# Optimization experiments

Hardware: AMD Instinct MI355X
Metric: run time of the kernel (lower is better)

## Reference

```python
import jax, jax.numpy as jnp
import numpy as np

N_NODES = 100000
N_EDGES = 1600000
IN_CH = 128
OUT_CH = 16
HEADS = 4
HID = HEADS * OUT_CH  # 64
OUT_SIZE = 4
NEG_SLOPE = 0.2


def _xavier(key, shape, fan_in, fan_out):
    bound = float(np.sqrt(6.0 / (fan_in + fan_out)))
    return jax.random.uniform(key, shape, jnp.float32, -bound, bound)


def setup_inputs() -> dict:
    key = jax.random.key(0)
    ks = jax.random.split(key, 32)
    inp = {
        "x": jax.random.normal(ks[0], (N_NODES, IN_CH), jnp.float32),
        "edge_index": jax.random.randint(ks[1], (2, N_EDGES), 0, N_NODES, jnp.int64),
    }
    cin = IN_CH
    for l in range(4):
        inp[f"W{l}"] = _xavier(ks[2 + 3 * l], (HID, cin), cin, HID)
        inp[f"b{l}"] = jnp.zeros((HID,), jnp.float32)
        inp[f"a{l}"] = _xavier(ks[3 + 3 * l], (HEADS, 2 * OUT_CH), 2 * OUT_CH, 1)
        cin = HID
    inp["fcW"] = _xavier(ks[20], (OUT_SIZE, HID), HID, OUT_SIZE)
    inp["fcb"] = jnp.zeros((OUT_SIZE,), jnp.float32)
    return inp


def _gat_layer(x, src, dst, W, b, att):
    n = x.shape[0]
    h = (x @ W.T + b).reshape(n, HEADS, OUT_CH)  # [N,H,C]
    # cat([x_i,x_j]) . att == (x_i . att[:, :C]) + (x_j . att[:, C:])
    si = jnp.einsum("nhc,hc->nh", h, att[:, :OUT_CH])  # target part
    sj = jnp.einsum("nhc,hc->nh", h, att[:, OUT_CH:])  # source part
    alpha = jax.nn.leaky_relu(si[dst] + sj[src], NEG_SLOPE)  # [E,H]
    deg = jax.ops.segment_sum(jnp.ones((src.shape[0],), x.dtype), dst, num_segments=n)
    alpha = alpha / deg[dst][:, None]
    msg = h[src] * alpha[:, :, None]  # [E,H,C]
    out = jax.ops.segment_sum(msg, dst, num_segments=n)  # [N,H,C]
    return out.reshape(n, HID)


def reference(x, edge_index, W0, b0, a0, W1, b1, a1, W2, b2, a2, W3, b3, a3, fcW, fcb):
    src = edge_index[0]  # x_j
    dst = edge_index[1]  # x_i (aggregation targets)
    for W, b, a in ((W0, b0, a0), (W1, b1, a1), (W2, b2, a2), (W3, b3, a3)):
        x = _gat_layer(x, src, dst, W, b, a)
    return x @ fcW.T + fcb
```

## Files before the change

kernel.cpp:

```cpp
#include <hip/hip_runtime.h>

#define NNODES 100000
#define NEDGES 1600000
#define IN_CH 128
#define HID 64
#define HEADS 4
#define OUT_CH 16
#define OUT_SIZE 4
#define NEG_SLOPE 0.2f
#define NXCD 8
#define CAP 64
#define CAP_SHIFT 6
#define UNR 8

__global__ __launch_bounds__(256, 4) void k_prep(
        const int* __restrict__ src, const int* __restrict__ dst,
        int* __restrict__ cursor, int* __restrict__ slots, int E, int rng, int nslot,
        const float* __restrict__ x, const float* __restrict__ W,
        const float* __restrict__ bias, const float* __restrict__ att,
        float* __restrict__ h, float* __restrict__ si, float* __restrict__ sj,
        int nlin, int n) {
    const int grp40 = blockIdx.x / 40;
    const int r40   = blockIdx.x % 40;

    if (r40 < 32) {
        const int slotId = grp40 * 32 + r40;
        if (slotId >= nslot) return;
        const int range = slotId & (NXCD - 1);
        const int chunk = slotId >> 3;
        const int lo = range * rng, hi = lo + rng;
        const int base = chunk * 2048 + threadIdx.x;
        #pragma unroll
        for (int i = 0; i < 8; ++i) {
            int e = base + i * 256;
            if (e < E) {
                int d = dst[e];
                if (d >= lo && d < hi) {
                    int pos = atomicAdd(&cursor[d], 1);
                    if (pos < CAP) slots[((size_t)d << CAP_SHIFT) + pos] = src[e];
                }
            }
        }
        return;
    }

    const int linId = grp40 * 8 + (r40 - 32);
    if (linId >= nlin) return;

    constexpr int IN = IN_CH;
    constexpr int BM = 64, BK = 64;
    constexpr int LDK = BK + 16;
    constexpr int LDB = HID + 4;
    __shared__ float As[BM][LDK];
    __shared__ float Bs[BK][LDB];

    const int tid = threadIdx.x;
    const int node0 = linId * BM;
    const int g = tid >> 4;
    const int v = tid & 15;
    const int tn = v * 4;

    float acc[4][4] = {};
    float4 ra[4], rb[4];

    #pragma unroll
    for (int i = 0; i < 4; ++i) {
        int m = g + 16 * i;
        int gm = node0 + m;
        ra[i] = make_float4(0.f, 0.f, 0.f, 0.f);
        if (gm < n) ra[i] = *reinterpret_cast<const float4*>(&x[(size_t)gm * IN + tn]);
        rb[i] = *reinterpret_cast<const float4*>(&W[(size_t)m * IN + tn]);
    }

    #pragma unroll
    for (int kk = 0; kk < IN; kk += BK) {
        #pragma unroll
        for (int i = 0; i < 4; ++i) {
            int m = g + 16 * i;
            *reinterpret_cast<float4*>(&As[m][tn]) = ra[i];
            Bs[tn + 0][m] = rb[i].x; Bs[tn + 1][m] = rb[i].y;
            Bs[tn + 2][m] = rb[i].z; Bs[tn + 3][m] = rb[i].w;
        }
        __syncthreads();
        if (kk + BK < IN) {
            #pragma unroll
            for (int i = 0; i < 4; ++i) {
                int m = g + 16 * i;
                int gm = node0 + m;
                ra[i] = make_float4(0.f, 0.f, 0.f, 0.f);
                if (gm < n)
                    ra[i] = *reinterpret_cast<const float4*>(&x[(size_t)gm * IN + kk + BK + tn]);
                rb[i] = *reinterpret_cast<const float4*>(&W[(size_t)m * IN + kk + BK + tn]);
            }
        }
        #pragma unroll
        for (int k4 = 0; k4 < BK; k4 += 4) {
            float4 b0 = *reinterpret_cast<const float4*>(&Bs[k4 + 0][tn]);
            float4 b1 = *reinterpret_cast<const float4*>(&Bs[k4 + 1][tn]);
            float4 b2 = *reinterpret_cast<const float4*>(&Bs[k4 + 2][tn]);
            float4 b3 = *reinterpret_cast<const float4*>(&Bs[k4 + 3][tn]);
            #pragma unroll
            for (int r = 0; r < 4; ++r) {
                float4 a = *reinterpret_cast<const float4*>(&As[g + 16 * r][k4]);
                acc[r][0] = fmaf(a.x, b0.x, acc[r][0]);
                acc[r][1] = fmaf(a.x, b0.y, acc[r][1]);
                acc[r][2] = fmaf(a.x, b0.z, acc[r][2]);
                acc[r][3] = fmaf(a.x, b0.w, acc[r][3]);
                acc[r][0] = fmaf(a.y, b1.x, acc[r][0]);
                acc[r][1] = fmaf(a.y, b1.y, acc[r][1]);
                acc[r][2] = fmaf(a.y, b1.z, acc[r][2]);
                acc[r][3] = fmaf(a.y, b1.w, acc[r][3]);
                acc[r][0] = fmaf(a.z, b2.x, acc[r][0]);
                acc[r][1] = fmaf(a.z, b2.y, acc[r][1]);
                acc[r][2] = fmaf(a.z, b2.z, acc[r][2]);
                acc[r][3] = fmaf(a.z, b2.w, acc[r][3]);
                acc[r][0] = fmaf(a.w, b3.x, acc[r][0]);
                acc[r][1] = fmaf(a.w, b3.y, acc[r][1]);
                acc[r][2] = fmaf(a.w, b3.z, acc[r][2]);
                acc[r][3] = fmaf(a.w, b3.w, acc[r][3]);
            }
        }
        __syncthreads();
    }

    float4 bb = *reinterpret_cast<const float4*>(&bias[tn]);
    #pragma unroll
    for (int r = 0; r < 4; ++r) {
        acc[r][0] += bb.x; acc[r][1] += bb.y; acc[r][2] += bb.z; acc[r][3] += bb.w;
        int gm = node0 + g + 16 * r;
        if (gm < n)
            *reinterpret_cast<float4*>(&h[(size_t)gm * HID + tn]) =
                make_float4(acc[r][0], acc[r][1], acc[r][2], acc[r][3]);
    }

    const int head = v >> 2;
    const int cl = (v & 3) * 4;
    const float* arow = att + head * (2 * OUT_CH);
    float pi[4], pj[4];
    #pragma unroll
    for (int r = 0; r < 4; ++r) {
        float vi = 0.f, vj = 0.f;
        #pragma unroll
        for (int c = 0; c < 4; ++c) {
            vi = fmaf(acc[r][c], arow[cl + c], vi);
            vj = fmaf(acc[r][c], arow[OUT_CH + cl + c], vj);
        }
        pi[r] = vi + __shfl_xor(vi, 1); pi[r] += __shfl_xor(pi[r], 2);
        pj[r] = vj + __shfl_xor(vj, 1); pj[r] += __shfl_xor(pj[r], 2);
    }
    {
        int r = v & 3;
        int gm = node0 + g + 16 * r;
        if (gm < n) {
            float siv = (r == 0) ? pi[0] : (r == 1) ? pi[1] : (r == 2) ? pi[2] : pi[3];
            float sjv = (r == 0) ? pj[0] : (r == 1) ? pj[1] : (r == 2) ? pj[2] : pj[3];
            si[gm * HEADS + head] = siv;
            sj[gm * HEADS + head] = sjv;
        }
    }
}

__global__ __launch_bounds__(256) void k_gather_lin(const int* __restrict__ slots,
                        const int* __restrict__ deg,
                        const float* __restrict__ h, const float* __restrict__ si,
                        const float* __restrict__ sj,
                        const float* __restrict__ Wn, const float* __restrict__ bn,
                        const float* __restrict__ attn,
                        float* __restrict__ h_out, float* __restrict__ si_out,
                        float* __restrict__ sj_out, int n) {
    __shared__ float Ws[HID][HID + 1];
    __shared__ float orow[16][HID + 4];
    __shared__ int   sl[16][CAP];

    const int tid  = threadIdx.x;
    const int lane = tid & 63;
    const int l16  = lane & 15;
    const int head = l16 >> 2;
    const int grp  = tid >> 4;
    const int node = blockIdx.x * 16 + grp;
    const bool active = node < n;

    #pragma unroll
    for (int i = 0; i < 4; ++i) {
        int f = tid + i * 256;
        int c = f >> 4;
        int k4 = (f & 15) * 4;
        float4 w = *reinterpret_cast<const float4*>(&Wn[(size_t)c * HID + k4]);
        Ws[k4 + 0][c] = w.x; Ws[k4 + 1][c] = w.y;
        Ws[k4 + 2][c] = w.z; Ws[k4 + 3][c] = w.w;
    }
    __syncthreads();

    int end = 0;
    float sid = 0.f, invd = 0.f;
    if (active) {
        int dg = deg[node];
        end = (dg < CAP ? dg : CAP);
        sid = si[node * HEADS + head];
        if (dg > 0) invd = 1.0f / (float)dg;
        int4 svv = *reinterpret_cast<const int4*>(&slots[((size_t)node << CAP_SHIFT) + l16 * 4]);
        *reinterpret_cast<int4*>(&sl[grp][l16 * 4]) = svv;
    }

    float4 acc = make_float4(0.f, 0.f, 0.f, 0.f);
    int j = 0;
    while (j < end) {
        float a[UNR];
        float4 hv[UNR];
        #pragma unroll
        for (int u = 0; u < UNR; ++u) {
            bool p = (j + u) < end;
            int idx = p ? j + u : 0;
            int s = sl[grp][idx];
            float e = sj[s * HEADS + head];
            hv[u] = *reinterpret_cast<const float4*>(&h[(size_t)s * HID + (l16 << 2)]);
            float av = sid + e;
            av = (av > 0.f) ? av : av * NEG_SLOPE;
            a[u] = p ? av : 0.f;
        }
        #pragma unroll
        for (int u = 0; u < UNR; ++u) {
            acc.x = fmaf(hv[u].x, a[u], acc.x);
            acc.y = fmaf(hv[u].y, a[u], acc.y);
            acc.z = fmaf(hv[u].z, a[u], acc.z);
            acc.w = fmaf(hv[u].w, a[u], acc.w);
        }
        j += UNR;
    }

    if (active) {
        acc.x *= invd; acc.y *= invd; acc.z *= invd; acc.w *= invd;
        *reinterpret_cast<float4*>(&orow[grp][l16 << 2]) = acc;

        const int c0 = l16 << 2;
        float4 hb = *reinterpret_cast<const float4*>(&bn[c0]);
        float h0 = hb.x, h1 = hb.y, h2 = hb.z, h3 = hb.w;
        #pragma unroll
        for (int k = 0; k < HID; ++k) {
            float o = orow[grp][k];
            float4 w = *reinterpret_cast<const float4*>(&Ws[k][c0]);
            h0 = fmaf(o, w.x, h0);
            h1 = fmaf(o, w.y, h1);
            h2 = fmaf(o, w.z, h2);
            h3 = fmaf(o, w.w, h3);
        }
        *reinterpret_cast<float4*>(&h_out[(size_t)node * HID + c0]) =
            make_float4(h0, h1, h2, h3);

        const int cl = (l16 & 3) * 4;
        const float* arow = attn + head * (2 * OUT_CH);
        float hv4[4] = {h0, h1, h2, h3};
        float vi = 0.f, vj = 0.f;
        #pragma unroll
        for (int c = 0; c < 4; ++c) {
            vi = fmaf(hv4[c], arow[cl + c], vi);
            vj = fmaf(hv4[c], arow[OUT_CH + cl + c], vj);
        }
        vi += __shfl_xor(vi, 1); vi += __shfl_xor(vi, 2);
        vj += __shfl_xor(vj, 1); vj += __shfl_xor(vj, 2);
        if ((l16 & 3) == 0) {
            si_out[node * HEADS + head] = vi;
            sj_out[node * HEADS + head] = vj;
        }
    }
}

__global__ __launch_bounds__(256) void k_gather_fc(const int* __restrict__ slots,
                        const int* __restrict__ deg,
                        const float* __restrict__ h, const float* __restrict__ si,
                        const float* __restrict__ sj,
                        const float* __restrict__ fcW, const float* __restrict__ fcb,
                        float* __restrict__ dout, int n) {
    __shared__ int sl[16][CAP];
    const int lane = threadIdx.x & 63;
    const int l16  = lane & 15;
    const int head = l16 >> 2;
    const int grp  = threadIdx.x >> 4;
    const int node = blockIdx.x * 16 + grp;
    const bool active = node < n;

    int end = 0;
    float sid = 0.f, invd = 0.f;
    if (active) {
        int dg = deg[node];
        end = (dg < CAP ? dg : CAP);
        sid = si[node * HEADS + head];
        if (dg > 0) invd = 1.0f / (float)dg;
        int4 svv = *reinterpret_cast<const int4*>(&slots[((size_t)node << CAP_SHIFT) + l16 * 4]);
        *reinterpret_cast<int4*>(&sl[grp][l16 * 4]) = svv;
    }

    float4 acc = make_float4(0.f, 0.f, 0.f, 0.f);
    int j = 0;
    while (j < end) {
        float a[UNR];
        float4 hv[UNR];
        #pragma unroll
        for (int u = 0; u < UNR; ++u) {
            bool p = (j + u) < end;
            int idx = p ? j + u : 0;
            int s = sl[grp][idx];
            float e = sj[s * HEADS + head];
            hv[u] = *reinterpret_cast<const float4*>(&h[(size_t)s * HID + (l16 << 2)]);
            float av = sid + e;
            av = (av > 0.f) ? av : av * NEG_SLOPE;
            a[u] = p ? av : 0.f;
        }
        #pragma unroll
        for (int u = 0; u < UNR; ++u) {
            acc.x = fmaf(hv[u].x, a[u], acc.x);
            acc.y = fmaf(hv[u].y, a[u], acc.y);
            acc.z = fmaf(hv[u].z, a[u], acc.z);
            acc.w = fmaf(hv[u].w, a[u], acc.w);
        }
        j += UNR;
    }
    if (active) {
        acc.x *= invd; acc.y *= invd; acc.z *= invd; acc.w *= invd;
        const int c0 = l16 << 2;
        float po[OUT_SIZE];
        #pragma unroll
        for (int o = 0; o < OUT_SIZE; ++o) {
            const float* wr = fcW + o * HID + c0;
            float p = acc.x * wr[0];
            p = fmaf(acc.y, wr[1], p);
            p = fmaf(acc.z, wr[2], p);
            p = fmaf(acc.w, wr[3], p);
            p += __shfl_xor(p, 1);
            p += __shfl_xor(p, 2);
            p += __shfl_xor(p, 4);
            p += __shfl_xor(p, 8);
            po[o] = p;
        }
        if (l16 < OUT_SIZE) {
            float val = (l16 == 0) ? po[0] : (l16 == 1) ? po[1]
                      : (l16 == 2) ? po[2] : po[3];
            dout[(size_t)node * OUT_SIZE + l16] = val + fcb[l16];
        }
    }
}

extern "C" void kernel_launch(void* const* d_in, const int* in_sizes, int n_in,
                              void* d_out, int out_size, void* d_ws, size_t ws_size,
                              hipStream_t stream) {
    const float* x0   = (const float*)d_in[0];
    const int*   ei   = (const int*)d_in[1];
    const int E = in_sizes[1] / 2;
    const int N = in_sizes[0] / IN_CH;
    const int* srcp = ei;
    const int* dstp = ei + E;

    const float* W[4] = {(const float*)d_in[2], (const float*)d_in[5], (const float*)d_in[8],  (const float*)d_in[11]};
    const float* B[4] = {(const float*)d_in[3], (const float*)d_in[6], (const float*)d_in[9],  (const float*)d_in[12]};
    const float* A[4] = {(const float*)d_in[4], (const float*)d_in[7], (const float*)d_in[10], (const float*)d_in[13]};
    const float* fcW = (const float*)d_in[14];
    const float* fcb = (const float*)d_in[15];

    float* ws    = (float*)d_ws;
    float* hA    = ws;
    float* hB    = hA  + (size_t)N * HID;
    float* siA   = hB  + (size_t)N * HID;
    float* sjA   = siA + (size_t)N * HEADS;
    float* siB   = sjA + (size_t)N * HEADS;
    float* sjB   = siB + (size_t)N * HEADS;
    int*   cursor= (int*)(sjB + (size_t)N * HEADS);
    int*   slots = cursor + N;

    const int rng = (N + NXCD - 1) / NXCD;
    hipMemsetAsync(cursor, 0, (size_t)N * sizeof(int), stream);

    const int nchunk = (E + 2047) / 2048;
    const int nslot  = nchunk * NXCD;
    const int nlin   = (N + 63) / 64;
    const int ngroups = ((nslot + 31) / 32 > (nlin + 7) / 8) ? (nslot + 31) / 32
                                                             : (nlin + 7) / 8;
    k_prep<<<ngroups * 40, 256, 0, stream>>>(srcp, dstp, cursor, slots, E, rng, nslot,
                                             x0, W[0], B[0], A[0], hA, siA, sjA, nlin, N);

    const int gblk = (N + 15) / 16;
    k_gather_lin<<<gblk, 256, 0, stream>>>(slots, cursor, hA, siA, sjA,
                                           W[1], B[1], A[1], hB, siB, sjB, N);
    k_gather_lin<<<gblk, 256, 0, stream>>>(slots, cursor, hB, siB, sjB,
                                           W[2], B[2], A[2], hA, siA, sjA, N);
    k_gather_lin<<<gblk, 256, 0, stream>>>(slots, cursor, hA, siA, sjA,
                                           W[3], B[3], A[3], hB, siB, sjB, N);
    k_gather_fc<<<gblk, 256, 0, stream>>>(slots, cursor, hB, siB, sjB,
                                          fcW, fcb, (float*)d_out, N);
}
```

Measured before the change: 387.0 us.

## Project last layer through fc per head before the final gather

The fc weights are applied to the layer-3 features inside the third gather kernel, producing per-head partial projections of 16 floats per node instead of 64 hidden features. The final gather then aggregates these scalars per head with the attention weights and reduces across heads. This reorders linear operations to shrink the random-access gather traffic of the last aggregation. It adds a few shuffles and alters floating-point summation order.

```diff
diff --git a/kernel.cpp b/kernel.cpp
--- a/kernel.cpp
+++ b/kernel.cpp
@@ -160,12 +160,13 @@
     }
 }
 
+template<int LAST>
 __global__ __launch_bounds__(256) void k_gather_lin(const int* __restrict__ slots,
                         const int* __restrict__ deg,
                         const float* __restrict__ h, const float* __restrict__ si,
                         const float* __restrict__ sj,
                         const float* __restrict__ Wn, const float* __restrict__ bn,
-                        const float* __restrict__ attn,
+                        const float* __restrict__ attn, const float* __restrict__ fcW,
                         float* __restrict__ h_out, float* __restrict__ si_out,
                         float* __restrict__ sj_out, int n) {
     __shared__ float Ws[HID][HID + 1];
@@ -244,8 +245,26 @@
             h2 = fmaf(o, w.z, h2);
             h3 = fmaf(o, w.w, h3);
         }
-        *reinterpret_cast<float4*>(&h_out[(size_t)node * HID + c0]) =
-            make_float4(h0, h1, h2, h3);
+        if (!LAST) {
+            *reinterpret_cast<float4*>(&h_out[(size_t)node * HID + c0]) =
+                make_float4(h0, h1, h2, h3);
+        } else {
+            float pp[OUT_SIZE];
+            #pragma unroll
+            for (int o = 0; o < OUT_SIZE; ++o) {
+                const float* wr = fcW + o * HID + c0;
+                float p = h0 * wr[0];
+                p = fmaf(h1, wr[1], p);
+                p = fmaf(h2, wr[2], p);
+                p = fmaf(h3, wr[3], p);
+                p += __shfl_xor(p, 1);
+                p += __shfl_xor(p, 2);
+                pp[o] = p;
+            }
+            int o = l16 & 3;
+            float val = (o == 0) ? pp[0] : (o == 1) ? pp[1] : (o == 2) ? pp[2] : pp[3];
+            h_out[(size_t)node * 16 + head * 4 + o] = val;
+        }
 
         const int cl = (l16 & 3) * 4;
         const float* arow = attn + head * (2 * OUT_CH);
@@ -265,11 +284,10 @@
     }
 }
 
-__global__ __launch_bounds__(256) void k_gather_fc(const int* __restrict__ slots,
+__global__ __launch_bounds__(256) void k_gather_fc2(const int* __restrict__ slots,
                         const int* __restrict__ deg,
-                        const float* __restrict__ h, const float* __restrict__ si,
-                        const float* __restrict__ sj,
-                        const float* __restrict__ fcW, const float* __restrict__ fcb,
+                        const float* __restrict__ hp, const float* __restrict__ si,
+                        const float* __restrict__ sj, const float* __restrict__ fcb,
                         float* __restrict__ dout, int n) {
     __shared__ int sl[16][CAP];
     const int lane = threadIdx.x & 63;
@@ -290,53 +308,31 @@
         *reinterpret_cast<int4*>(&sl[grp][l16 * 4]) = svv;
     }
 
-    float4 acc = make_float4(0.f, 0.f, 0.f, 0.f);
+    float acc = 0.f;
     int j = 0;
     while (j < end) {
         float a[UNR];
-        float4 hv[UNR];
+        float hv[UNR];
         #pragma unroll
         for (int u = 0; u < UNR; ++u) {
             bool p = (j + u) < end;
             int idx = p ? j + u : 0;
             int s = sl[grp][idx];
             float e = sj[s * HEADS + head];
-            hv[u] = *reinterpret_cast<const float4*>(&h[(size_t)s * HID + (l16 << 2)]);
+            hv[u] = hp[(size_t)s * 16 + l16];
             float av = sid + e;
             av = (av > 0.f) ? av : av * NEG_SLOPE;
             a[u] = p ? av : 0.f;
         }
         #pragma unroll
-        for (int u = 0; u < UNR; ++u) {
-            acc.x = fmaf(hv[u].x, a[u], acc.x);
-            acc.y = fmaf(hv[u].y, a[u], acc.y);
-            acc.z = fmaf(hv[u].z, a[u], acc.z);
-            acc.w = fmaf(hv[u].w, a[u], acc.w);
-        }
+        for (int u = 0; u < UNR; ++u) acc = fmaf(hv[u], a[u], acc);
         j += UNR;
     }
     if (active) {
-        acc.x *= invd; acc.y *= invd; acc.z *= invd; acc.w *= invd;
-        const int c0 = l16 << 2;
-        float po[OUT_SIZE];
-        #pragma unroll
-        for (int o = 0; o < OUT_SIZE; ++o) {
-            const float* wr = fcW + o * HID + c0;
-            float p = acc.x * wr[0];
-            p = fmaf(acc.y, wr[1], p);
-            p = fmaf(acc.z, wr[2], p);
-            p = fmaf(acc.w, wr[3], p);
-            p += __shfl_xor(p, 1);
-            p += __shfl_xor(p, 2);
-            p += __shfl_xor(p, 4);
-            p += __shfl_xor(p, 8);
-            po[o] = p;
-        }
-        if (l16 < OUT_SIZE) {
-            float val = (l16 == 0) ? po[0] : (l16 == 1) ? po[1]
-                      : (l16 == 2) ? po[2] : po[3];
-            dout[(size_t)node * OUT_SIZE + l16] = val + fcb[l16];
-        }
+        acc += __shfl_xor(acc, 4);
+        acc += __shfl_xor(acc, 8);
+        if (l16 < OUT_SIZE)
+            dout[(size_t)node * OUT_SIZE + l16] = acc * invd + fcb[l16];
     }
 }
 
@@ -378,12 +374,12 @@
                                              x0, W[0], B[0], A[0], hA, siA, sjA, nlin, N);
 
     const int gblk = (N + 15) / 16;
-    k_gather_lin<<<gblk, 256, 0, stream>>>(slots, cursor, hA, siA, sjA,
-                                           W[1], B[1], A[1], hB, siB, sjB, N);
-    k_gather_lin<<<gblk, 256, 0, stream>>>(slots, cursor, hB, siB, sjB,
-                                           W[2], B[2], A[2], hA, siA, sjA, N);
-    k_gather_lin<<<gblk, 256, 0, stream>>>(slots, cursor, hA, siA, sjA,
-                                           W[3], B[3], A[3], hB, siB, sjB, N);
-    k_gather_fc<<<gblk, 256, 0, stream>>>(slots, cursor, hB, siB, sjB,
-                                          fcW, fcb, (float*)d_out, N);
+    k_gather_lin<0><<<gblk, 256, 0, stream>>>(slots, cursor, hA, siA, sjA,
+                                              W[1], B[1], A[1], nullptr, hB, siB, sjB, N);
+    k_gather_lin<0><<<gblk, 256, 0, stream>>>(slots, cursor, hB, siB, sjB,
+                                              W[2], B[2], A[2], nullptr, hA, siA, sjA, N);
+    k_gather_lin<1><<<gblk, 256, 0, stream>>>(slots, cursor, hA, siA, sjA,
+                                              W[3], B[3], A[3], fcW, hB, siB, sjB, N);
+    k_gather_fc2<<<gblk, 256, 0, stream>>>(slots, cursor, hB, siB, sjB,
+                                           fcb, (float*)d_out, N);
 }
```

Result: faster. 348.4 us (-10.0%).
